# Kernel optimization log

Hardware: AMD Instinct MI355X
Metric: run time of the kernel (lower is better)

Reference implementation:

```python
import jax, jax.numpy as jnp
import numpy as np

N = 4096        # batch nodes
E = 65536       # random edges (self-loops appended -> 69632 total)
F_IN = 256
H = 128
C = 2
MIN = 1024      # minority (class 1) count; first MIN nodes
REP = 2         # int(N_pct/100) synthetic reps per minority sample


def setup_inputs() -> dict:
    key = jax.random.key(0)
    ks = jax.random.split(key, 24)
    feat = jax.random.normal(ks[0], (N, F_IN), dtype=jnp.float32)
    src = jax.random.randint(ks[1], (E,), 0, N, dtype=jnp.int32)
    dst = jax.random.randint(ks[2], (E,), 0, N, dtype=jnp.int32)
    loops = jnp.arange(N, dtype=jnp.int32)
    src = jnp.concatenate([src, loops])
    dst = jnp.concatenate([dst, loops])
    # dense batch adjacency (target for EdgeLoss), A[i,j]=1 if edge j->i
    adj = jnp.zeros((N, N), dtype=jnp.float32).at[dst, src].set(1.0)
    # deterministic labels: first MIN nodes are minority class 1
    labels = jnp.concatenate([jnp.ones((MIN,), jnp.int32), jnp.zeros((N - MIN,), jnp.int32)])

    def w(k, shape, fan_in):
        return jax.random.normal(k, shape, dtype=jnp.float32) / np.sqrt(fan_in)

    params = dict(
        W_pool0=w(ks[3], (F_IN, F_IN), F_IN), b_pool0=jnp.zeros((F_IN,), jnp.float32),
        W_self0=w(ks[4], (H, F_IN), F_IN), W_neigh0=w(ks[5], (H, F_IN), F_IN), b0=jnp.zeros((H,), jnp.float32),
        W_pool1=w(ks[6], (H, H), H), b_pool1=jnp.zeros((H,), jnp.float32),
        W_self1=w(ks[7], (H, H), H), W_neigh1=w(ks[8], (H, H), H), b1=jnp.zeros((H,), jnp.float32),
        de_weight=jax.random.uniform(ks[9], (H, H), jnp.float32, -1.0 / np.sqrt(H), 1.0 / np.sqrt(H)),
        W_conv=w(ks[10], (H, 2 * H), 2 * H),
        W_clf=w(ks[11], (C, H), H), b_clf=jnp.zeros((C,), jnp.float32),
        gaps=jax.random.uniform(ks[12], (MIN, REP), jnp.float32),  # SMOTE interpolation gaps
    )
    return dict(feat=feat, adj=adj, src=src, dst=dst, labels=labels, **params)


def _sage_pool_layer(h, src, dst, W_pool, b_pool, W_self, W_neigh, b):
    # DGL SAGEConv aggregator_type='pool': max over neighbors of relu(fc_pool(h))
    p = jax.nn.relu(h @ W_pool.T + b_pool)                     # [N, d]
    hn = jax.ops.segment_max(p[src], dst, num_segments=h.shape[0])
    hn = jnp.where(jnp.isfinite(hn), hn, 0.0)
    return h @ W_self.T + hn @ W_neigh.T + b


def _l2norm(x, eps=1e-12):
    return x / jnp.maximum(jnp.linalg.norm(x, axis=1, keepdims=True), eps)


def _smote_nn_interp(cand, gaps):
    # pairwise euclidean distances (vectorized form of the per-row loop)
    sq = jnp.sum(cand * cand, axis=1)
    d2 = sq[:, None] + sq[None, :] - 2.0 * (cand @ cand.T)
    dist = jnp.sqrt(jnp.maximum(d2, 0.0))
    nn_idx = jnp.argsort(dist, axis=1)[:, 1]                   # k=2 -> single nearest (excl. self)
    diff = cand[nn_idx] - cand                                  # [MIN, H]
    synth = cand[:, None, :] + gaps[:, :, None] * diff[:, None, :]  # [MIN, REP, H], i-major order
    return synth.reshape(MIN * REP, cand.shape[1])


def reference(feat, adj, src, dst, labels,
              W_pool0, b_pool0, W_self0, W_neigh0, b0,
              W_pool1, b_pool1, W_self1, W_neigh1, b1,
              de_weight, W_conv, W_clf, b_clf, gaps):
    # ---- Encoder (2 SAGEConv 'pool' layers; dropout is eval-mode identity) ----
    h = _sage_pool_layer(feat, src, dst, W_pool0, b_pool0, W_self0, W_neigh0, b0)
    h = _l2norm(jax.nn.relu(h))
    h = _sage_pool_layer(h, src, dst, W_pool1, b_pool1, W_self1, W_neigh1, b1)
    # ---- SMOTE (minority = first MIN rows, by deterministic label construction) ----
    synth = _smote_nn_interp(h[:MIN], gaps)
    x = jnp.concatenate([h, synth], axis=0)                    # [N + MIN*REP, H]
    y = jnp.concatenate([labels, jnp.ones((MIN * REP,), jnp.int32)])
    # ---- Decoder: sigmoid(out @ out.T) ----
    out = x @ de_weight.T
    pred_adj = jax.nn.sigmoid(out @ out.T)                     # [6144, 6144]
    # ---- EdgeLoss vs dense batch adjacency ----
    rec = pred_adj[:N, :N]
    edge_num = jnp.sum(adj != 0).astype(jnp.float32)
    neg_w = edge_num / (float(N * N) - edge_num)
    weight = jnp.where(adj == 0, neg_w, 1.0)
    loss = jnp.sum(weight * (rec - adj) ** 2)
    # ---- threshold + SageClassifier (1 layer, no activation before clf) ----
    pred_adj = jnp.where(pred_adj >= 0.5, pred_adj, 0.0)
    neigh = (pred_adj @ x) / (jnp.sum(pred_adj, axis=1, keepdims=True) + 1.0)
    hc = jnp.concatenate([x, neigh], axis=-1) @ W_conv.T
    logits = hc @ W_clf.T + b_clf                              # [6144, 2]
    return logits, y, loss
```

## Files before the change

kernel.cpp:

```cpp
#include <hip/hip_runtime.h>
#include <cstddef>

typedef unsigned short ushort_t;
typedef __attribute__((ext_vector_type(8))) short bf16x8;
typedef __attribute__((ext_vector_type(4))) float f32x4;
typedef __attribute__((ext_vector_type(16))) float f32x16;

#define WS_P0     0u
#define WS_DOTS   0u
#define WS_OBK    524288u
#define WS_HN0    1048576u
#define WS_HC     1048576u
#define WS_H1     2097152u
#define WS_H1N    2621440u
#define WS_P1     3145728u
#define WS_PVB    3145728u
#define WS_HN1    3670016u
#define WS_H2     4194304u
#define WS_X      4718592u
#define WS_BITMAP 5767168u
#define WS_NEIGH  6291456u
#define WS_ROWSUM 7077888u
#define WS_SCAL   7084032u
#define WS_DEG    7084048u
#define WS_NN     7088144u
#define WS_CUR    7089168u
#define WS_ROWPTR 7093264u
#define WS_EIDX   7097361u

__device__ inline ushort_t f2bf(float f) {
  unsigned u = __float_as_uint(f);
  u += 0x7fff + ((u >> 16) & 1);
  return (ushort_t)(u >> 16);
}
__device__ inline float bf2f(ushort_t h) {
  return __uint_as_float((unsigned)h << 16);
}

__global__ __launch_bounds__(256, 2) void mgemm(
    const float* __restrict__ A, int lda,
    const float* __restrict__ B, int ldb,
    const float* __restrict__ A2, int lda2,
    const float* __restrict__ B2, int ldb2,
    const float* __restrict__ bias,
    float* __restrict__ C, int ldc,
    int K, int relu,
    ushort_t* __restrict__ Cb,
    const float* __restrict__ a2scale,
    const float* __restrict__ Ahi)
{
  __shared__ ushort_t AhS[64][36], AlS[64][36], BhS[64][36], BlS[64][36];
  const int tid = threadIdx.x;
  const int lane = tid & 63;
  const int w = tid >> 6;
  const int lo = lane & 31, hi = lane >> 5;
  const int iq = (w & 1) << 5, jq = (w >> 1) << 5;
  const int i0 = blockIdx.y << 6, j0 = blockIdx.x << 6;
  const int lr = tid >> 2;
  const int c8 = (tid & 3) << 3;
  f32x16 acc;
#pragma unroll
  for (int t = 0; t < 16; ++t) acc[t] = 0.f;
  const int npass = (A2 != nullptr) ? 2 : 1;
  for (int pass = 0; pass < npass; ++pass) {
    const float* Ap = pass ? A2 : A; const int la = pass ? lda2 : lda;
    const float* Bp = pass ? B2 : B; const int lb = pass ? ldb2 : ldb;
    const float* Arow = (pass == 0 && Ahi != nullptr && (i0 + lr) >= 4096)
        ? (Ahi + (size_t)(i0 + lr - 4096) * la)
        : (Ap + (size_t)(i0 + lr) * la);
    const float* Brow = Bp + (size_t)(j0 + lr) * lb;
    const float sc = (pass && a2scale) ? __frcp_rn(a2scale[i0 + lr] + 1.f) : 1.f;
    for (int k0 = 0; k0 < K; k0 += 32) {
      float av[8], bv[8];
      {
        const float4 a0 = *(const float4*)(Arow + k0 + c8);
        const float4 a1 = *(const float4*)(Arow + k0 + c8 + 4);
        const float4 b0 = *(const float4*)(Brow + k0 + c8);
        const float4 b1 = *(const float4*)(Brow + k0 + c8 + 4);
        av[0]=a0.x*sc; av[1]=a0.y*sc; av[2]=a0.z*sc; av[3]=a0.w*sc;
        av[4]=a1.x*sc; av[5]=a1.y*sc; av[6]=a1.z*sc; av[7]=a1.w*sc;
        bv[0]=b0.x; bv[1]=b0.y; bv[2]=b0.z; bv[3]=b0.w;
        bv[4]=b1.x; bv[5]=b1.y; bv[6]=b1.z; bv[7]=b1.w;
      }
      __syncthreads();
      {
        ushort_t ah8[8], al8[8], bh8[8], bl8[8];
#pragma unroll
        for (int e = 0; e < 8; ++e) {
          const ushort_t ah = f2bf(av[e]);
          ah8[e] = ah; al8[e] = f2bf(av[e] - bf2f(ah));
          const ushort_t bh = f2bf(bv[e]);
          bh8[e] = bh; bl8[e] = f2bf(bv[e] - bf2f(bh));
        }
        *(bf16x8*)&AhS[lr][c8] = *(bf16x8*)ah8;
        *(bf16x8*)&AlS[lr][c8] = *(bf16x8*)al8;
        *(bf16x8*)&BhS[lr][c8] = *(bf16x8*)bh8;
        *(bf16x8*)&BlS[lr][c8] = *(bf16x8*)bl8;
      }
      __syncthreads();
#pragma unroll
      for (int kk = 0; kk < 32; kk += 16) {
        const bf16x8 ahf = *(const bf16x8*)&AhS[iq + lo][kk + (hi << 3)];
        const bf16x8 alf = *(const bf16x8*)&AlS[iq + lo][kk + (hi << 3)];
        const bf16x8 bhf = *(const bf16x8*)&BhS[jq + lo][kk + (hi << 3)];
        const bf16x8 blf = *(const bf16x8*)&BlS[jq + lo][kk + (hi << 3)];
        acc = __builtin_amdgcn_mfma_f32_32x32x16_bf16(ahf, bhf, acc, 0, 0, 0);
        acc = __builtin_amdgcn_mfma_f32_32x32x16_bf16(alf, bhf, acc, 0, 0, 0);
        acc = __builtin_amdgcn_mfma_f32_32x32x16_bf16(ahf, blf, acc, 0, 0, 0);
      }
    }
  }
  const int col = j0 + jq + lo;
  const float badd = bias ? bias[col] : 0.f;
#pragma unroll
  for (int t = 0; t < 16; ++t) {
    float o = acc[t] + badd;
    if (relu) o = fmaxf(o, 0.f);
    const int row = i0 + iq + (t & 3) + ((t >> 2) << 3) + (hi << 2);
    if (Cb) {
      const size_t off = ((size_t)(row >> 5) << 12) +
          (size_t)(((col >> 4) << 9) +
                   (((((col >> 3) & 1) << 5) + (row & 31)) << 3) + (col & 7));
      Cb[off] = f2bf(o);
    } else {
      C[(size_t)row * ldc + col] = o;
    }
  }
}

__global__ void count_bitmap_k(const int* __restrict__ src, const int* __restrict__ dst,
                               int* __restrict__ deg, unsigned* __restrict__ bitmap, int E) {
  const int e = blockIdx.x * 256 + threadIdx.x;
  if (e < E) {
    const int d_ = dst[e], s_ = src[e];
    atomicAdd(&deg[d_], 1);
    const unsigned cell = ((unsigned)d_ << 12) + (unsigned)s_;
    atomicOr(&bitmap[cell >> 5], 1u << (cell & 31));
  }
}

__global__ __launch_bounds__(1024) void scan_k(const int* __restrict__ deg,
                                               int* __restrict__ rowptr,
                                               int* __restrict__ cursor) {
  __shared__ int sums[1024];
  const int t = threadIdx.x;
  const int4 d = *(const int4*)(deg + (t << 2));
  const int local = d.x + d.y + d.z + d.w;
  sums[t] = local;
  __syncthreads();
  for (int off = 1; off < 1024; off <<= 1) {
    int v = (t >= off) ? sums[t - off] : 0;
    __syncthreads();
    sums[t] += v;
    __syncthreads();
  }
  const int excl = sums[t] - local;
  const int o0 = excl, o1 = o0 + d.x, o2 = o1 + d.y, o3 = o2 + d.z;
  rowptr[(t<<2)+0]=o0; rowptr[(t<<2)+1]=o1; rowptr[(t<<2)+2]=o2; rowptr[(t<<2)+3]=o3;
  cursor[(t<<2)+0]=o0; cursor[(t<<2)+1]=o1; cursor[(t<<2)+2]=o2; cursor[(t<<2)+3]=o3;
  if (t == 1023) rowptr[4096] = sums[1023];
}

__global__ void fill_k(const int* __restrict__ src, const int* __restrict__ dst,
                       int* __restrict__ cursor, int* __restrict__ eidx, int E) {
  const int e = blockIdx.x * 256 + threadIdx.x;
  if (e < E) {
    const int p = atomicAdd(&cursor[dst[e]], 1);
    eidx[p] = src[e];
  }
}

__global__ void segmax_k(const float* __restrict__ p, const int* __restrict__ rowptr,
                         const int* __restrict__ eidx, float* __restrict__ hn, int F) {
  const int row = blockIdx.x, f = threadIdx.x;
  const int b = rowptr[row], e = rowptr[row + 1];
  float m = 0.f;
  for (int k = b; k < e; ++k) m = fmaxf(m, p[(size_t)eidx[k] * F + f]);
  hn[(size_t)row * F + f] = m;
}

__device__ inline float wave_sum(float v) {
#pragma unroll
  for (int o = 32; o > 0; o >>= 1) v += __shfl_down(v, o, 64);
  return v;
}

__global__ void relu_l2norm_k(const float* __restrict__ in, float* __restrict__ out) {
  const int row = blockIdx.x, f = threadIdx.x;
  const float v = fmaxf(in[(size_t)row * 128 + f], 0.f);
  const float ss = wave_sum(v * v);
  __shared__ float w[2];
  if ((f & 63) == 0) w[f >> 6] = ss;
  __syncthreads();
  const float denom = fmaxf(sqrtf(w[0] + w[1]), 1e-12f);
  out[(size_t)row * 128 + f] = v / denom;
}

__global__ void argmin_k(const float* __restrict__ dots, int* __restrict__ nn) {
  __shared__ float sqd[1024];
  const int i = blockIdx.x, tid = threadIdx.x;
#pragma unroll
  for (int z = 0; z < 4; ++z) {
    const int j = (tid << 2) + z;
    sqd[j] = dots[(size_t)j * 1025];
  }
  __syncthreads();
  float best = 3.402823466e38f; int bidx = 0x7fffffff;
  const float si = sqd[i];
  for (int j = tid; j < 1024; j += 256) {
    if (j == i) continue;
    float d2 = si + sqd[j] - 2.f * dots[(size_t)i * 1024 + j];
    d2 = fmaxf(d2, 0.f);
    if (d2 < best || (d2 == best && j < bidx)) { best = d2; bidx = j; }
  }
  __shared__ float bv[256]; __shared__ int bi[256];
  bv[tid] = best; bi[tid] = bidx;
  __syncthreads();
  for (int s = 128; s > 0; s >>= 1) {
    if (tid < s) {
      if (bv[tid+s] < bv[tid] || (bv[tid+s] == bv[tid] && bi[tid+s] < bi[tid])) {
        bv[tid] = bv[tid+s]; bi[tid] = bi[tid+s];
      }
    }
    __syncthreads();
  }
  if (tid == 0) nn[i] = bi[0];
}

__global__ __launch_bounds__(256) void build_pack_k(
    const float* __restrict__ h2, const int* __restrict__ nn,
    const float* __restrict__ gaps, float* __restrict__ synth,
    ushort_t* __restrict__ pvb) {
  __shared__ ushort_t s[4096];
  const int jt = blockIdx.x, tid = threadIdx.x;
  if (jt < 128) {
    const float* ip = h2 + ((size_t)jt << 12);
#pragma unroll
    for (int k = 0; k < 4; ++k) {
      const float4 v = *(const float4*)(ip + (tid << 4) + (k << 2));
      ushort4 h; h.x = f2bf(v.x); h.y = f2bf(v.y); h.z = f2bf(v.z); h.w = f2bf(v.w);
      *(ushort4*)(s + (tid << 4) + (k << 2)) = h;
    }
  } else {
    const int row = tid >> 3;
    const int sIdx = ((jt - 128) << 5) + row;
    const int i = sIdx >> 1;
    const float g = gaps[sIdx];
    const int ni = nn[i];
#pragma unroll
    for (int k = 0; k < 4; ++k) {
      const int f = ((tid & 7) << 4) + (k << 2);
      const float4 c4 = *(const float4*)(h2 + (size_t)i * 128 + f);
      const float4 n4 = *(const float4*)(h2 + (size_t)ni * 128 + f);
      float4 v;
      v.x = c4.x + g * (n4.x - c4.x);
      v.y = c4.y + g * (n4.y - c4.y);
      v.z = c4.z + g * (n4.z - c4.z);
      v.w = c4.w + g * (n4.w - c4.w);
      *(float4*)(synth + (size_t)sIdx * 128 + f) = v;
      ushort4 h; h.x = f2bf(v.x); h.y = f2bf(v.y); h.z = f2bf(v.z); h.w = f2bf(v.w);
      *(ushort4*)(s + (row << 7) + f) = h;
    }
  }
  __syncthreads();
  const int u = tid & 31, ft = (tid >> 5) & 3, cc = tid >> 7;
  ushort_t* op = pvb + ((size_t)jt << 12) + (cc << 11) + (ft << 9);
#pragma unroll
  for (int m = 0; m < 2; ++m) {
    const int l = (u << 1) + m;
    const int f = (ft << 5) + (l & 31);
    const int jb = (cc << 4) + ((l >> 5) << 3);
    ushort4 o0, o1;
    o0.x = s[(jb + 0) * 128 + f]; o0.y = s[(jb + 1) * 128 + f];
    o0.z = s[(jb + 2) * 128 + f]; o0.w = s[(jb + 3) * 128 + f];
    o1.x = s[(jb + 4) * 128 + f]; o1.y = s[(jb + 5) * 128 + f];
    o1.z = s[(jb + 6) * 128 + f]; o1.w = s[(jb + 7) * 128 + f];
    *(ushort4*)(op + (l << 3) + 0) = o0;
    *(ushort4*)(op + (l << 3) + 4) = o1;
  }
}

__global__ __launch_bounds__(256, 2) void fused_mfma(
    const ushort_t* __restrict__ obk,
    const ushort_t* __restrict__ pvb,
    const unsigned* __restrict__ bitmap,
    float* __restrict__ neigh,
    float* __restrict__ rowsum,
    float* __restrict__ scal)
{
  __shared__ float wred[4][4];
  const int tid = threadIdx.x;
  const int w = tid >> 6;
  const int lane = tid & 63;
  const int lo = lane & 31, hi = lane >> 5;
  const int it = (blockIdx.x << 2) + w;
  const int iw = it << 5;
  const int jt0 = blockIdx.y << 4;
  const bool loss_i = (it < 128);

  bf16x8 qf[8];
  {
    const ushort_t* qp = obk + ((size_t)it << 12) + (lane << 3);
#pragma unroll
    for (int c = 0; c < 8; ++c) qf[c] = *(const bf16x8*)(qp + (c << 9));
  }
  f32x16 oacc[4];
#pragma unroll
  for (int ft = 0; ft < 4; ++ft)
#pragma unroll
    for (int r = 0; r < 16; ++r) oacc[ft][r] = 0.f;
  float rs = 0.f, s_all = 0.f, s1a = 0.f, suba = 0.f, ecf = 0.f;

  bf16x8 a[8];
  {
    const ushort_t* kp = obk + ((size_t)jt0 << 12) + (lane << 3);
#pragma unroll
    for (int c = 0; c < 8; ++c) a[c] = *(const bf16x8*)(kp + (c << 9));
  }

  for (int t = 0; t < 16; ++t) {
    const int jt = jt0 + t;
    f32x16 s0, s1;
#pragma unroll
    for (int r = 0; r < 16; ++r) { s0[r] = 0.f; s1[r] = 0.f; }
#pragma unroll
    for (int c = 0; c < 4; ++c) {
      s0 = __builtin_amdgcn_mfma_f32_32x32x16_bf16(a[c], qf[c], s0, 0, 0, 0);
      s1 = __builtin_amdgcn_mfma_f32_32x32x16_bf16(a[c + 4], qf[c + 4], s1, 0, 0, 0);
    }
    bf16x8 bvf[2][4];
    {
      const ushort_t* vp = pvb + ((size_t)jt << 12) + (lane << 3);
#pragma unroll
      for (int cc = 0; cc < 2; ++cc)
#pragma unroll
        for (int ft = 0; ft < 4; ++ft)
          bvf[cc][ft] = *(const bf16x8*)(vp + (cc << 11) + (ft << 9));
    }
    if (t < 15) {
      const ushort_t* kp = obk + ((size_t)(jt + 1) << 12) + (lane << 3);
#pragma unroll
      for (int c = 0; c < 8; ++c) a[c] = *(const bf16x8*)(kp + (c << 9));
    }
    const bool loss_t = loss_i && (jt < 128);
    unsigned word = 0u;
    if (loss_t) word = bitmap[((unsigned)(iw + lo) << 7) + (unsigned)jt];
    float p[16];
    if (loss_t) {
      ecf += (float)__popc(word & (0x0F0F0F0Fu << (hi << 2)));
#pragma unroll
      for (int r = 0; r < 16; ++r) {
        const float v = s0[r] + s1[r];
        const float sg = __builtin_amdgcn_rcpf(1.f + __expf(-v));
        const int jl = (r & 3) + ((r >> 2) << 3) + (hi << 2);
        const float e_ = (float)((word >> jl) & 1u);
        s_all += sg * sg;
        s1a  += e_ * (sg - 1.f) * (sg - 1.f);
        suba += e_ * sg * sg;
        const float tv = (v >= 0.f) ? sg : 0.f;
        p[r] = tv; rs += tv;
      }
    } else {
#pragma unroll
      for (int r = 0; r < 16; ++r) {
        const float v = s0[r] + s1[r];
        const float sg = __builtin_amdgcn_rcpf(1.f + __expf(-v));
        const float tv = (v >= 0.f) ? sg : 0.f;
        p[r] = tv; rs += tv;
      }
    }
#pragma unroll
    for (int cc = 0; cc < 2; ++cc) {
      const int b8 = cc << 3;
      unsigned c01, c23, c45, c67;
      asm("v_cvt_pk_bf16_f32 %0, %1, %2" : "=v"(c01) : "v"(p[b8+0]), "v"(p[b8+1]));
      asm("v_cvt_pk_bf16_f32 %0, %1, %2" : "=v"(c23) : "v"(p[b8+2]), "v"(p[b8+3]));
      asm("v_cvt_pk_bf16_f32 %0, %1, %2" : "=v"(c45) : "v"(p[b8+4]), "v"(p[b8+5]));
      asm("v_cvt_pk_bf16_f32 %0, %1, %2" : "=v"(c67) : "v"(p[b8+6]), "v"(p[b8+7]));
      const auto w0 = __builtin_amdgcn_permlane32_swap((int)c01, (int)c45, false, false);
      const auto w1 = __builtin_amdgcn_permlane32_swap((int)c23, (int)c67, false, false);
      union { int i[4]; bf16x8 h; } u;
      u.i[0] = w0[0]; u.i[1] = w1[0]; u.i[2] = w0[1]; u.i[3] = w1[1];
#pragma unroll
      for (int ft = 0; ft < 4; ++ft)
        oacc[ft] = __builtin_amdgcn_mfma_f32_32x32x16_bf16(u.h, bvf[cc][ft], oacc[ft], 0, 0, 0);
    }
  }
#pragma unroll
  for (int ft = 0; ft < 4; ++ft)
#pragma unroll
    for (int r = 0; r < 16; ++r) {
      const int ir = (r & 3) + ((r >> 2) << 3) + (hi << 2);
      atomicAdd(&neigh[(size_t)(iw + ir) * 128 + (ft << 5) + lo], oacc[ft][r]);
    }
  rs += __shfl_xor(rs, 32, 64);
  if (hi == 0) atomicAdd(&rowsum[iw + lo], rs);
  {
    float v0 = wave_sum(s_all), v1 = wave_sum(s1a), v2 = wave_sum(suba), v3 = wave_sum(ecf);
    if (lane == 0) { wred[w][0] = v0; wred[w][1] = v1; wred[w][2] = v2; wred[w][3] = v3; }
  }
  __syncthreads();
  if (tid < 4) {
    const float t = wred[0][tid] + wred[1][tid] + wred[2][tid] + wred[3][tid];
    const int dst = (tid == 0) ? 0 : (tid == 1) ? 1 : (tid == 2) ? 3 : 4;
    atomicAdd(&scal[dst], t);
  }
}

__global__ void logits_y_loss_k(const float* __restrict__ hc, const float* __restrict__ Wclf,
                                const float* __restrict__ bclf, const int* __restrict__ labels,
                                const float* __restrict__ scal,
                                float* __restrict__ outp) {
  const int i = blockIdx.x, f = threadIdx.x;
  const float h = hc[(size_t)i * 128 + f];
  const float v0 = wave_sum(h * Wclf[f]);
  const float v1 = wave_sum(h * Wclf[128 + f]);
  __shared__ float w0[2], w1[2];
  if ((f & 63) == 0) { w0[f >> 6] = v0; w1[f >> 6] = v1; }
  __syncthreads();
  if (f == 0) {
    outp[(size_t)i * 2 + 0] = w0[0] + w0[1] + bclf[0];
    outp[(size_t)i * 2 + 1] = w1[0] + w1[1] + bclf[1];
    outp[12288 + i] = (i < 4096) ? (float)labels[i] : 1.f;
    if (i == 0) {
      const float cnt = scal[4];
      const float neg_w = cnt / (16777216.f - cnt);
      outp[18432] = neg_w * (scal[0] - scal[3]) + scal[1];
    }
  }
}

extern "C" void kernel_launch(void* const* d_in, const int* in_sizes, int n_in,
                              void* d_out, int out_size, void* d_ws, size_t ws_size,
                              hipStream_t stream) {
  const float* feat     = (const float*)d_in[0];
  const int*   src      = (const int*)d_in[2];
  const int*   dst      = (const int*)d_in[3];
  const int*   labels   = (const int*)d_in[4];
  const float* W_pool0  = (const float*)d_in[5];
  const float* b_pool0  = (const float*)d_in[6];
  const float* W_self0  = (const float*)d_in[7];
  const float* W_neigh0 = (const float*)d_in[8];
  const float* b0       = (const float*)d_in[9];
  const float* W_pool1  = (const float*)d_in[10];
  const float* b_pool1  = (const float*)d_in[11];
  const float* W_self1  = (const float*)d_in[12];
  const float* W_neigh1 = (const float*)d_in[13];
  const float* b1       = (const float*)d_in[14];
  const float* de_w     = (const float*)d_in[15];
  const float* W_conv   = (const float*)d_in[16];
  const float* W_clf    = (const float*)d_in[17];
  const float* b_clf    = (const float*)d_in[18];
  const float* gaps     = (const float*)d_in[19];
  const int E = in_sizes[2];

  float* ws = (float*)d_ws;
  float* p0       = ws + WS_P0;
  float* dots     = ws + WS_DOTS;
  ushort_t* obk   = (ushort_t*)(ws + WS_OBK);
  float* hn0      = ws + WS_HN0;
  float* hc       = ws + WS_HC;
  unsigned* bitmap= (unsigned*)(ws + WS_BITMAP);
  float* h1       = ws + WS_H1;
  float* h1n      = ws + WS_H1N;
  float* p1       = ws + WS_P1;
  ushort_t* pvb   = (ushort_t*)(ws + WS_PVB);
  float* hn1      = ws + WS_HN1;
  float* h2       = ws + WS_H2;
  float* synth    = ws + WS_X;
  float* neigh    = ws + WS_NEIGH;
  float* rowsum   = ws + WS_ROWSUM;
  float* scal     = ws + WS_SCAL;
  int* deg        = (int*)(ws + WS_DEG);
  int* nn         = (int*)(ws + WS_NN);
  int* cursor     = (int*)(ws + WS_CUR);
  int* rowptr     = (int*)(ws + WS_ROWPTR);
  int* eidx       = (int*)(ws + WS_EIDX);

  float* outp = (float*)d_out;
  const dim3 blk(256);

  hipMemsetAsync(bitmap, 0, (size_t)(WS_DEG + 4096 - WS_BITMAP) * 4, stream);

  count_bitmap_k<<<(E + 255) / 256, blk, 0, stream>>>(src, dst, deg, bitmap, E);
  scan_k<<<1, 1024, 0, stream>>>(deg, rowptr, cursor);
  fill_k<<<(E + 255) / 256, blk, 0, stream>>>(src, dst, cursor, eidx, E);

  mgemm<<<dim3(4, 64), blk, 0, stream>>>(feat, 256, W_pool0, 256,
                                         nullptr, 0, nullptr, 0,
                                         b_pool0, p0, 256, 256, 1, nullptr, nullptr, nullptr);
  segmax_k<<<4096, 256, 0, stream>>>(p0, rowptr, eidx, hn0, 256);
  mgemm<<<dim3(2, 64), blk, 0, stream>>>(feat, 256, W_self0, 256,
                                         hn0, 256, W_neigh0, 256,
                                         b0, h1, 128, 256, 0, nullptr, nullptr, nullptr);
  relu_l2norm_k<<<4096, 128, 0, stream>>>(h1, h1n);

  mgemm<<<dim3(2, 64), blk, 0, stream>>>(h1n, 128, W_pool1, 128,
                                         nullptr, 0, nullptr, 0,
                                         b_pool1, p1, 128, 128, 1, nullptr, nullptr, nullptr);
  segmax_k<<<4096, 128, 0, stream>>>(p1, rowptr, eidx, hn1, 128);
  mgemm<<<dim3(2, 64), blk, 0, stream>>>(h1n, 128, W_self1, 128,
                                         hn1, 128, W_neigh1, 128,
                                         b1, h2, 128, 128, 0, nullptr, nullptr, nullptr);

  mgemm<<<dim3(16, 16), blk, 0, stream>>>(h2, 128, h2, 128,
                                          nullptr, 0, nullptr, 0,
                                          nullptr, dots, 1024, 128, 0, nullptr, nullptr, nullptr);
  argmin_k<<<1024, 256, 0, stream>>>(dots, nn);
  build_pack_k<<<192, blk, 0, stream>>>(h2, nn, gaps, synth, pvb);

  mgemm<<<dim3(2, 96), blk, 0, stream>>>(h2, 128, de_w, 128,
                                         nullptr, 0, nullptr, 0,
                                         nullptr, nullptr, 0, 128, 0, obk, nullptr, synth);
  fused_mfma<<<dim3(48, 12), blk, 0, stream>>>(obk, pvb, bitmap, neigh, rowsum, scal);

  mgemm<<<dim3(2, 96), blk, 0, stream>>>(h2, 128, W_conv, 256,
                                         neigh, 128, W_conv + 128, 256,
                                         nullptr, hc, 128, 128, 0, nullptr, rowsum, synth);
  logits_y_loss_k<<<6144, 128, 0, stream>>>(hc, W_clf, b_clf, labels, scal, outp);

  (void)n_in; (void)out_size; (void)ws_size; (void)in_sizes;
}
```

Baseline: 312.0 us.

## Fuse classifier into conv GEMM epilogue and store pool activations as bf16

The final logits projection is folded into the last mgemm epilogue: each block reduces its tile against W_clf with wave shuffles and atomically adds into the output, which build_pack_k pre-initialises with the bias and labels. This drops one kernel launch and the round trip of the hc intermediate. Separately, the pool GEMMs now write bf16 row-major output, and segmax reads the bf16 values, roughly halving gather traffic. The cost is rounding error in the max-pool inputs and nondeterministic float atomics in the logits.

```diff
diff --git a/kernel.cpp b/kernel.cpp
--- a/kernel.cpp
+++ b/kernel.cpp
@@ -10,7 +10,6 @@
 #define WS_DOTS   0u
 #define WS_OBK    524288u
 #define WS_HN0    1048576u
-#define WS_HC     1048576u
 #define WS_H1     2097152u
 #define WS_H1N    2621440u
 #define WS_P1     3145728u
@@ -47,7 +46,11 @@
     int K, int relu,
     ushort_t* __restrict__ Cb,
     const float* __restrict__ a2scale,
-    const float* __restrict__ Ahi)
+    const float* __restrict__ Ahi,
+    int cbplain,
+    const float* __restrict__ Wclf,
+    const float* __restrict__ scal4,
+    float* __restrict__ outp)
 {
   __shared__ ushort_t AhS[64][36], AlS[64][36], BhS[64][36], BlS[64][36];
   const int tid = threadIdx.x;
@@ -111,6 +114,29 @@
     }
   }
   const int col = j0 + jq + lo;
+  if (Wclf) {
+    const float w0c = Wclf[col], w1c = Wclf[128 + col];
+#pragma unroll
+    for (int t = 0; t < 16; ++t) {
+      float q0 = acc[t] * w0c, q1 = acc[t] * w1c;
+#pragma unroll
+      for (int m = 1; m < 32; m <<= 1) {
+        q0 += __shfl_xor(q0, m, 64);
+        q1 += __shfl_xor(q1, m, 64);
+      }
+      if (lo == 0) {
+        const int row = i0 + iq + (t & 3) + ((t >> 2) << 3) + (hi << 2);
+        atomicAdd(&outp[(size_t)row * 2 + 0], q0);
+        atomicAdd(&outp[(size_t)row * 2 + 1], q1);
+      }
+    }
+    if (blockIdx.x == 0 && blockIdx.y == 0 && tid == 0) {
+      const float cnt = scal4[4];
+      const float neg_w = cnt / (16777216.f - cnt);
+      outp[18432] = neg_w * (scal4[0] - scal4[3]) + scal4[1];
+    }
+    return;
+  }
   const float badd = bias ? bias[col] : 0.f;
 #pragma unroll
   for (int t = 0; t < 16; ++t) {
@@ -118,10 +144,14 @@
     if (relu) o = fmaxf(o, 0.f);
     const int row = i0 + iq + (t & 3) + ((t >> 2) << 3) + (hi << 2);
     if (Cb) {
-      const size_t off = ((size_t)(row >> 5) << 12) +
-          (size_t)(((col >> 4) << 9) +
-                   (((((col >> 3) & 1) << 5) + (row & 31)) << 3) + (col & 7));
-      Cb[off] = f2bf(o);
+      if (cbplain) {
+        Cb[(size_t)row * ldc + col] = f2bf(o);
+      } else {
+        const size_t off = ((size_t)(row >> 5) << 12) +
+            (size_t)(((col >> 4) << 9) +
+                     (((((col >> 3) & 1) << 5) + (row & 31)) << 3) + (col & 7));
+        Cb[off] = f2bf(o);
+      }
     } else {
       C[(size_t)row * ldc + col] = o;
     }
@@ -170,12 +200,12 @@
   }
 }
 
-__global__ void segmax_k(const float* __restrict__ p, const int* __restrict__ rowptr,
-                         const int* __restrict__ eidx, float* __restrict__ hn, int F) {
+__global__ void segmax_bf_k(const ushort_t* __restrict__ p, const int* __restrict__ rowptr,
+                            const int* __restrict__ eidx, float* __restrict__ hn, int F) {
   const int row = blockIdx.x, f = threadIdx.x;
   const int b = rowptr[row], e = rowptr[row + 1];
   float m = 0.f;
-  for (int k = b; k < e; ++k) m = fmaxf(m, p[(size_t)eidx[k] * F + f]);
+  for (int k = b; k < e; ++k) m = fmaxf(m, bf2f(p[(size_t)eidx[k] * F + f]));
   hn[(size_t)row * F + f] = m;
 }
 
@@ -230,9 +260,17 @@
 __global__ __launch_bounds__(256) void build_pack_k(
     const float* __restrict__ h2, const int* __restrict__ nn,
     const float* __restrict__ gaps, float* __restrict__ synth,
-    ushort_t* __restrict__ pvb) {
+    ushort_t* __restrict__ pvb,
+    const int* __restrict__ labels, const float* __restrict__ bclf,
+    float* __restrict__ outp) {
   __shared__ ushort_t s[4096];
   const int jt = blockIdx.x, tid = threadIdx.x;
+  if (tid < 32) {
+    const int i = (jt << 5) + tid;
+    outp[(size_t)i * 2 + 0] = bclf[0];
+    outp[(size_t)i * 2 + 1] = bclf[1];
+    outp[12288 + i] = (i < 4096) ? (float)labels[i] : 1.f;
+  }
   if (jt < 128) {
     const float* ip = h2 + ((size_t)jt << 12);
 #pragma unroll
@@ -404,29 +442,6 @@
     const float t = wred[0][tid] + wred[1][tid] + wred[2][tid] + wred[3][tid];
     const int dst = (tid == 0) ? 0 : (tid == 1) ? 1 : (tid == 2) ? 3 : 4;
     atomicAdd(&scal[dst], t);
-  }
-}
-
-__global__ void logits_y_loss_k(const float* __restrict__ hc, const float* __restrict__ Wclf,
-                                const float* __restrict__ bclf, const int* __restrict__ labels,
-                                const float* __restrict__ scal,
-                                float* __restrict__ outp) {
-  const int i = blockIdx.x, f = threadIdx.x;
-  const float h = hc[(size_t)i * 128 + f];
-  const float v0 = wave_sum(h * Wclf[f]);
-  const float v1 = wave_sum(h * Wclf[128 + f]);
-  __shared__ float w0[2], w1[2];
-  if ((f & 63) == 0) { w0[f >> 6] = v0; w1[f >> 6] = v1; }
-  __syncthreads();
-  if (f == 0) {
-    outp[(size_t)i * 2 + 0] = w0[0] + w0[1] + bclf[0];
-    outp[(size_t)i * 2 + 1] = w1[0] + w1[1] + bclf[1];
-    outp[12288 + i] = (i < 4096) ? (float)labels[i] : 1.f;
-    if (i == 0) {
-      const float cnt = scal[4];
-      const float neg_w = cnt / (16777216.f - cnt);
-      outp[18432] = neg_w * (scal[0] - scal[3]) + scal[1];
-    }
   }
 }
 
@@ -455,15 +470,14 @@
   const int E = in_sizes[2];
 
   float* ws = (float*)d_ws;
-  float* p0       = ws + WS_P0;
+  ushort_t* p0b   = (ushort_t*)(ws + WS_P0);
   float* dots     = ws + WS_DOTS;
   ushort_t* obk   = (ushort_t*)(ws + WS_OBK);
   float* hn0      = ws + WS_HN0;
-  float* hc       = ws + WS_HC;
   unsigned* bitmap= (unsigned*)(ws + WS_BITMAP);
   float* h1       = ws + WS_H1;
   float* h1n      = ws + WS_H1N;
-  float* p1       = ws + WS_P1;
+  ushort_t* p1b   = (ushort_t*)(ws + WS_P1);
   ushort_t* pvb   = (ushort_t*)(ws + WS_PVB);
   float* hn1      = ws + WS_HN1;
   float* h2       = ws + WS_H2;
@@ -488,36 +502,42 @@
 
   mgemm<<<dim3(4, 64), blk, 0, stream>>>(feat, 256, W_pool0, 256,
                                          nullptr, 0, nullptr, 0,
-                                         b_pool0, p0, 256, 256, 1, nullptr, nullptr, nullptr);
-  segmax_k<<<4096, 256, 0, stream>>>(p0, rowptr, eidx, hn0, 256);
+                                         b_pool0, nullptr, 256, 256, 1, p0b, nullptr, nullptr,
+                                         1, nullptr, nullptr, nullptr);
+  segmax_bf_k<<<4096, 256, 0, stream>>>(p0b, rowptr, eidx, hn0, 256);
   mgemm<<<dim3(2, 64), blk, 0, stream>>>(feat, 256, W_self0, 256,
                                          hn0, 256, W_neigh0, 256,
-                                         b0, h1, 128, 256, 0, nullptr, nullptr, nullptr);
+                                         b0, h1, 128, 256, 0, nullptr, nullptr, nullptr,
+                                         0, nullptr, nullptr, nullptr);
   relu_l2norm_k<<<4096, 128, 0, stream>>>(h1, h1n);
 
   mgemm<<<dim3(2, 64), blk, 0, stream>>>(h1n, 128, W_pool1, 128,
                                          nullptr, 0, nullptr, 0,
-                                         b_pool1, p1, 128, 128, 1, nullptr, nullptr, nullptr);
-  segmax_k<<<4096, 128, 0, stream>>>(p1, rowptr, eidx, hn1, 128);
+                                         b_pool1, nullptr, 128, 128, 1, p1b, nullptr, nullptr,
+                                         1, nullptr, nullptr, nullptr);
+  segmax_bf_k<<<4096, 128, 0, stream>>>(p1b, rowptr, eidx, hn1, 128);
   mgemm<<<dim3(2, 64), blk, 0, stream>>>(h1n, 128, W_self1, 128,
                                          hn1, 128, W_neigh1, 128,
-                                         b1, h2, 128, 128, 0, nullptr, nullptr, nullptr);
+                                         b1, h2, 128, 128, 0, nullptr, nullptr, nullptr,
+                                         0, nullptr, nullptr, nullptr);
 
   mgemm<<<dim3(16, 16), blk, 0, stream>>>(h2, 128, h2, 128,
                                           nullptr, 0, nullptr, 0,
-                                          nullptr, dots, 1024, 128, 0, nullptr, nullptr, nullptr);
+                                          nullptr, dots, 1024, 128, 0, nullptr, nullptr, nullptr,
+                                          0, nullptr, nullptr, nullptr);
   argmin_k<<<1024, 256, 0, stream>>>(dots, nn);
-  build_pack_k<<<192, blk, 0, stream>>>(h2, nn, gaps, synth, pvb);
+  build_pack_k<<<192, blk, 0, stream>>>(h2, nn, gaps, synth, pvb, labels, b_clf, outp);
 
   mgemm<<<dim3(2, 96), blk, 0, stream>>>(h2, 128, de_w, 128,
                                          nullptr, 0, nullptr, 0,
-                                         nullptr, nullptr, 0, 128, 0, obk, nullptr, synth);
+                                         nullptr, nullptr, 0, 128, 0, obk, nullptr, synth,
+                                         0, nullptr, nullptr, nullptr);
   fused_mfma<<<dim3(48, 12), blk, 0, stream>>>(obk, pvb, bitmap, neigh, rowsum, scal);
 
   mgemm<<<dim3(2, 96), blk, 0, stream>>>(h2, 128, W_conv, 256,
                                          neigh, 128, W_conv + 128, 256,
-                                         nullptr, hc, 128, 128, 0, nullptr, rowsum, synth);
-  logits_y_loss_k<<<6144, 128, 0, stream>>>(hc, W_clf, b_clf, labels, scal, outp);
+                                         nullptr, nullptr, 128, 128, 0, nullptr, rowsum, synth,
+                                         0, W_clf, scal, outp);
 
   (void)n_in; (void)out_size; (void)ws_size; (void)in_sizes;
 }
```

Result: no change. 308.0 us (-1.3%).
